# Optimization experiments

Measured on AMD Instinct MI355X. Metric: run time of the kernel, lower is better.

Reference implementation:

```python
import jax, jax.numpy as jnp
import numpy as np

Q_MAX = 127.0  # int8 symmetric quant range


def setup_inputs() -> dict:
    key = jax.random.key(0)
    kx, kw, ks = jax.random.split(key, 3)
    M, K, N = 16384, 4096, 4096
    x = jax.random.normal(kx, (M, K), dtype=jnp.float32)
    # int8 weight values in [-127, 127]
    weight = jax.random.randint(kw, (N, K), -127, 128, dtype=jnp.int32).astype(jnp.int8)
    # per-output-row dequant scale, small positive values as a real quantizer would produce
    weight_scale = jax.random.uniform(ks, (N, 1), dtype=jnp.float32, minval=1e-3, maxval=1e-2)
    return {"x": x, "weight": weight, "weight_scale": weight_scale}


def reference(x, weight, weight_scale):
    # --- per-token dynamic activation quantization (get_hip_quant(per_Token)) ---
    amax = jnp.max(jnp.abs(x), axis=-1, keepdims=True)            # [M,1]
    x_scale = amax / Q_MAX                                        # [M,1]
    x_q = jnp.clip(jnp.round(x / jnp.maximum(x_scale, 1e-8)), -Q_MAX, Q_MAX)  # int8 values, kept fp32
    # --- gemm_a8w8: int8xint8 GEMM with fused dequant (row scale_a * col scale_b) ---
    acc = jnp.einsum('mk,nk->mn', x_q, weight.astype(jnp.float32),
                     preferred_element_type=jnp.float32)          # [M,N] int accumulation in fp32
    y = acc * x_scale * weight_scale.T                            # fused dequant scales
    return y  # fp32 stand-in for otype=bf16 output
```

## Files before the change

### kernel.cpp

```cpp
#include <hip/hip_runtime.h>
#include <stdint.h>

#define M_DIM 16384
#define N_DIM 4096
#define K_DIM 4096

#define BM 256
#define BN 256
#define BK 128
#define NT (K_DIM / BK)

typedef int i32x4 __attribute__((ext_vector_type(4)));

__device__ __forceinline__ void async16(const uint8_t* g, uint8_t* l) {
    __builtin_amdgcn_global_load_lds(
        (const __attribute__((address_space(1))) void*)g,
        (__attribute__((address_space(3))) void*)l,
        16, 0, 0);
}

__global__ __launch_bounds__(256) void prep_kernel(const float* __restrict__ x,
                                                   const int* __restrict__ w32,
                                                   uint32_t* __restrict__ xq,
                                                   float* __restrict__ xscale,
                                                   uint32_t* __restrict__ w8) {
    const int b = blockIdx.x;
    const int t = threadIdx.x;
    if (b >= M_DIM) {
        const int i = (b - M_DIM) * 256 + t;
        const int4 v = reinterpret_cast<const int4*>(w32)[i];
        w8[i] = (uint32_t)(v.x & 255) | ((uint32_t)(v.y & 255) << 8) |
                ((uint32_t)(v.z & 255) << 16) | ((uint32_t)(v.w & 255) << 24);
        return;
    }
    const int m = b;
    const float4* row = reinterpret_cast<const float4*>(x + (size_t)m * K_DIM);
    float4 v[4];
    float amax = 0.0f;
#pragma unroll
    for (int i = 0; i < 4; ++i) {
        v[i] = row[t + i * 256];
        amax = fmaxf(amax, fmaxf(fmaxf(fabsf(v[i].x), fabsf(v[i].y)),
                                 fmaxf(fabsf(v[i].z), fabsf(v[i].w))));
    }
#pragma unroll
    for (int off = 32; off > 0; off >>= 1) amax = fmaxf(amax, __shfl_xor(amax, off));
    __shared__ float smax[4];
    if ((t & 63) == 0) smax[t >> 6] = amax;
    __syncthreads();
    amax = fmaxf(fmaxf(smax[0], smax[1]), fmaxf(smax[2], smax[3]));
    const float scale = amax / 127.0f;
    const float s = fmaxf(scale, 1e-8f);
    if (t == 0) xscale[m] = scale;
    uint32_t* orow = xq + (size_t)m * (K_DIM / 4);
#pragma unroll
    for (int i = 0; i < 4; ++i) {
        int q0 = __float2int_rn(v[i].x / s);
        int q1 = __float2int_rn(v[i].y / s);
        int q2 = __float2int_rn(v[i].z / s);
        int q3 = __float2int_rn(v[i].w / s);
        q0 = max(-127, min(127, q0));
        q1 = max(-127, min(127, q1));
        q2 = max(-127, min(127, q2));
        q3 = max(-127, min(127, q3));
        orow[t + i * 256] = (uint32_t)(q0 & 255) | ((uint32_t)(q1 & 255) << 8) |
                            ((uint32_t)(q2 & 255) << 16) | ((uint32_t)(q3 & 255) << 24);
    }
}

__global__ __launch_bounds__(512, 2) void gemm_kernel(
    const uint8_t* __restrict__ Aq, const float* __restrict__ ascale,
    const uint8_t* __restrict__ Bq, const float* __restrict__ wscale,
    float* __restrict__ out) {
    __shared__ uint8_t lds[4 * BM * BK];
    uint8_t* ldsA0 = lds;
    uint8_t* ldsA1 = lds + BM * BK;
    uint8_t* ldsB0 = lds + 2 * BM * BK;
    uint8_t* ldsB1 = lds + 3 * BM * BK;

    const int tid = threadIdx.x;
    const int lane = tid & 63;
    const int w = tid >> 6;
    const int wr = w >> 2;
    const int wc = w & 3;
    const int lr = lane & 15;
    const int lg = lane >> 4;

    const int bid = blockIdx.x;
    const int swz = (bid & 7) * (1024 / 8) + (bid >> 3);
    const size_t row0 = (size_t)(swz >> 4) * BM;
    const size_t col0 = (size_t)(swz & 15) * BN;
    const uint8_t* Ab = Aq + row0 * K_DIM;
    const uint8_t* Bb = Bq + col0 * K_DIM;

    i32x4 acc[8][4];
#pragma unroll
    for (int i = 0; i < 8; ++i)
#pragma unroll
        for (int j = 0; j < 4; ++j) acc[i][j] = (i32x4){0, 0, 0, 0};

#define STAGE_P(BASE, DST, KT)                                                   \
    do {                                                                         \
        _Pragma("unroll") for (int it_ = 0; it_ < 4; ++it_) {                    \
            const int idx_ = it_ * 512 + tid;                                    \
            const int m_ = idx_ >> 3, p_ = idx_ & 7;                             \
            async16((BASE) + (size_t)m_ * K_DIM + (KT) * BK +                    \
                        ((p_ ^ (m_ & 7)) << 4),                                  \
                    (DST) + (it_ * 512 + w * 64) * 16);                          \
        }                                                                        \
    } while (0)

#define READ_K(BUFA, BUFB, KK, F)                                                \
    do {                                                                         \
        _Pragma("unroll") for (int q_ = 0; q_ < 8; ++q_) {                       \
            const int r_ = wr * 128 + q_ * 16 + lr;                              \
            const int u_ = (KK) * 4 + lg;                                        \
            afk[F][q_] = *reinterpret_cast<const i32x4*>(                        \
                (BUFA) + r_ * BK + ((u_ ^ (r_ & 7)) << 4));                      \
        }                                                                        \
        _Pragma("unroll") for (int p_ = 0; p_ < 4; ++p_) {                       \
            const int r_ = wc * 64 + p_ * 16 + lr;                               \
            const int u_ = (KK) * 4 + lg;                                        \
            bfk[F][p_] = *reinterpret_cast<const i32x4*>(                        \
                (BUFB) + r_ * BK + ((u_ ^ (r_ & 7)) << 4));                      \
        }                                                                        \
    } while (0)

#define CLUSTER(F)                                                               \
    do {                                                                         \
        __builtin_amdgcn_s_setprio(1);                                           \
        _Pragma("unroll") for (int q_ = 0; q_ < 8; ++q_)                         \
        _Pragma("unroll") for (int p_ = 0; p_ < 4; ++p_)                         \
            acc[q_][p_] = __builtin_amdgcn_mfma_i32_16x16x64_i8(                 \
                afk[F][q_], bfk[F][p_], acc[q_][p_], 0, 0, 0);                   \
        __builtin_amdgcn_s_setprio(0);                                           \
    } while (0)

#define BAR __builtin_amdgcn_s_barrier()
#define VMCNT(N) asm volatile("s_waitcnt vmcnt(" #N ")" ::: "memory")
#define LGKM0                                              \
    do {                                                   \
        asm volatile("s_waitcnt lgkmcnt(0)" ::: "memory"); \
        __builtin_amdgcn_sched_barrier(0);                 \
    } while (0)

#define TILE_G0(CA, CB, NA, NB, TB, TA2)                                         \
    do {                                                                         \
        LGKM0;                                                  \
        STAGE_P(Bb, NB, TB);                                         \
        READ_K(CA, CB, 1, 1);                                            \
        CLUSTER(0);                                                              \
        LGKM0;                                                     \
        VMCNT(0);                                      \
        BAR;                                                                     \
        STAGE_P(Ab, CA, TA2);                               \
        READ_K(NA, NB, 0, 0);                                       \
        CLUSTER(1);                                                              \
    } while (0)

#define TILE_G1(CA, CB, NA, NB, TB, TA2)                                         \
    do {                                                                         \
        LGKM0;                                                                   \
        STAGE_P(Bb, NB, TB);                                                     \
        CLUSTER(0);                                                              \
        READ_K(CA, CB, 1, 1);                                                    \
        LGKM0;                                                                   \
        VMCNT(0);                                                                \
        BAR;                                                                     \
        STAGE_P(Ab, CA, TA2);                                                    \
        CLUSTER(1);                                                              \
        READ_K(NA, NB, 0, 0);                                                    \
    } while (0)

#define MAIN_LOOP(TILE_X)                                                        \
    do {                                                                         \
        READ_K(ldsA0, ldsB0, 0, 0);                                              \
        _Pragma("unroll 1") for (int it2 = 0; it2 < NT / 2; ++it2) {             \
            const int T = 2 * it2;                                               \
            const int Tp2 = (T + 2 < NT) ? T + 2 : NT - 1;                       \
            const int Tp3 = (T + 3 < NT) ? T + 3 : NT - 1;                       \
            TILE_X(ldsA0, ldsB0, ldsA1, ldsB1, T + 1, Tp2);                      \
            TILE_X(ldsA1, ldsB1, ldsA0, ldsB0, Tp2, Tp3);                        \
        }                                                                        \
    } while (0)

    i32x4 afk[2][8], bfk[2][4];

    STAGE_P(Ab, ldsA0, 0);
    STAGE_P(Bb, ldsB0, 0);
    STAGE_P(Ab, ldsA1, 1);
    VMCNT(4);
    BAR;

    if (wr == 0) {
        MAIN_LOOP(TILE_G0);
    } else {
        MAIN_LOOP(TILE_G1);
    }

    const float* asp = ascale + row0 + wr * 128;
    const float* wsp = wscale + col0 + wc * 64;
    float wsv[4];
#pragma unroll
    for (int nf = 0; nf < 4; ++nf) wsv[nf] = wsp[nf * 16 + lr];
    float* outBase = out + (row0 + wr * 128) * (size_t)N_DIM + col0 + wc * 64;
#pragma unroll
    for (int mf = 0; mf < 8; ++mf) {
#pragma unroll
        for (int j = 0; j < 4; ++j) {
            const int r = mf * 16 + lg * 4 + j;
            const float av = asp[r];
            float* orow = outBase + (size_t)r * N_DIM;
#pragma unroll
            for (int nf = 0; nf < 4; ++nf) {
                orow[nf * 16 + lr] = (float)acc[mf][nf][j] * av * wsv[nf];
            }
        }
    }
#undef STAGE_P
#undef READ_K
#undef CLUSTER
#undef TILE_G0
#undef TILE_G1
#undef MAIN_LOOP
#undef BAR
#undef VMCNT
#undef LGKM0
}

extern "C" void kernel_launch(void* const* d_in, const int* in_sizes, int n_in,
                              void* d_out, int out_size, void* d_ws, size_t ws_size,
                              hipStream_t stream) {
    const float* x = (const float*)d_in[0];
    const int* w32 = (const int*)d_in[1];
    const float* wscale = (const float*)d_in[2];
    float* out = (float*)d_out;

    uint8_t* ws = (uint8_t*)d_ws;
    uint32_t* xq = (uint32_t*)ws;
    float* xscale = (float*)(ws + (size_t)M_DIM * K_DIM);
    uint8_t* wq = ws + (size_t)M_DIM * K_DIM + (size_t)M_DIM * 4;

    prep_kernel<<<dim3(M_DIM + N_DIM * K_DIM / 4 / 256), 256, 0, stream>>>(
        x, w32, xq, xscale, (uint32_t*)wq);
    gemm_kernel<<<dim3((M_DIM / BM) * (N_DIM / BN)), 512, 0, stream>>>(
        (const uint8_t*)xq, xscale, wq, wscale, out);
}
```

Before: 341.6 us.

## Switch int8 GEMM to 32x32x32 MFMA tiles and drop redundant lgkm waits

Replaces the 16x16x64 int8 MFMA with the 32x32x32 variant, so each wave computes its 128x64 sub-tile as 4x2 32x32 blocks with 16-element accumulators. LDS fragment reads and the epilogue row/column mapping are rewritten to match the new MFMA register layout. It also removes the leading lgkmcnt(0) wait at the start of each tile stage. The larger instruction means fewer MFMA issues and fewer LDS fragment loads per K step. The cost is a changed output-store pattern, and a risk of LDS hazards from the removed wait.

```diff
diff --git a/kernel.cpp b/kernel.cpp
--- a/kernel.cpp
+++ b/kernel.cpp
@@ -11,6 +11,7 @@
 #define NT (K_DIM / BK)
 
 typedef int i32x4 __attribute__((ext_vector_type(4)));
+typedef int i32x16 __attribute__((ext_vector_type(16)));
 
 __device__ __forceinline__ void async16(const uint8_t* g, uint8_t* l) {
     __builtin_amdgcn_global_load_lds(
@@ -83,8 +84,8 @@
     const int w = tid >> 6;
     const int wr = w >> 2;
     const int wc = w & 3;
-    const int lr = lane & 15;
-    const int lg = lane >> 4;
+    const int l31 = lane & 31;
+    const int hi = lane >> 5;
 
     const int bid = blockIdx.x;
     const int swz = (bid & 7) * (1024 / 8) + (bid >> 3);
@@ -93,11 +94,11 @@
     const uint8_t* Ab = Aq + row0 * K_DIM;
     const uint8_t* Bb = Bq + col0 * K_DIM;
 
-    i32x4 acc[8][4];
-#pragma unroll
-    for (int i = 0; i < 8; ++i)
-#pragma unroll
-        for (int j = 0; j < 4; ++j) acc[i][j] = (i32x4){0, 0, 0, 0};
+    i32x16 acc[4][2];
+#pragma unroll
+    for (int i = 0; i < 4; ++i)
+#pragma unroll
+        for (int j = 0; j < 2; ++j) acc[i][j] = (i32x16)(0);
 
 #define STAGE_P(BASE, DST, KT)                                                   \
     do {                                                                         \
@@ -112,16 +113,18 @@
 
 #define READ_K(BUFA, BUFB, KK, F)                                                \
     do {                                                                         \
-        _Pragma("unroll") for (int q_ = 0; q_ < 8; ++q_) {                       \
-            const int r_ = wr * 128 + q_ * 16 + lr;                              \
-            const int u_ = (KK) * 4 + lg;                                        \
-            afk[F][q_] = *reinterpret_cast<const i32x4*>(                        \
+        _Pragma("unroll") for (int mf_ = 0; mf_ < 4; ++mf_)                      \
+        _Pragma("unroll") for (int s_ = 0; s_ < 2; ++s_) {                       \
+            const int r_ = wr * 128 + mf_ * 32 + l31;                            \
+            const int u_ = (KK) * 4 + s_ * 2 + hi;                               \
+            afk[F][mf_ * 2 + s_] = *reinterpret_cast<const i32x4*>(              \
                 (BUFA) + r_ * BK + ((u_ ^ (r_ & 7)) << 4));                      \
         }                                                                        \
-        _Pragma("unroll") for (int p_ = 0; p_ < 4; ++p_) {                       \
-            const int r_ = wc * 64 + p_ * 16 + lr;                               \
-            const int u_ = (KK) * 4 + lg;                                        \
-            bfk[F][p_] = *reinterpret_cast<const i32x4*>(                        \
+        _Pragma("unroll") for (int nh_ = 0; nh_ < 2; ++nh_)                      \
+        _Pragma("unroll") for (int s_ = 0; s_ < 2; ++s_) {                       \
+            const int r_ = wc * 64 + nh_ * 32 + l31;                             \
+            const int u_ = (KK) * 4 + s_ * 2 + hi;                               \
+            bfk[F][nh_ * 2 + s_] = *reinterpret_cast<const i32x4*>(              \
                 (BUFB) + r_ * BK + ((u_ ^ (r_ & 7)) << 4));                      \
         }                                                                        \
     } while (0)
@@ -129,10 +132,12 @@
 #define CLUSTER(F)                                                               \
     do {                                                                         \
         __builtin_amdgcn_s_setprio(1);                                           \
-        _Pragma("unroll") for (int q_ = 0; q_ < 8; ++q_)                         \
-        _Pragma("unroll") for (int p_ = 0; p_ < 4; ++p_)                         \
-            acc[q_][p_] = __builtin_amdgcn_mfma_i32_16x16x64_i8(                 \
-                afk[F][q_], bfk[F][p_], acc[q_][p_], 0, 0, 0);                   \
+        _Pragma("unroll") for (int s_ = 0; s_ < 2; ++s_)                         \
+        _Pragma("unroll") for (int mf_ = 0; mf_ < 4; ++mf_)                      \
+        _Pragma("unroll") for (int nh_ = 0; nh_ < 2; ++nh_)                      \
+            acc[mf_][nh_] = __builtin_amdgcn_mfma_i32_32x32x32_i8(               \
+                afk[F][mf_ * 2 + s_], bfk[F][nh_ * 2 + s_],                      \
+                acc[mf_][nh_], 0, 0, 0);                                         \
         __builtin_amdgcn_s_setprio(0);                                           \
     } while (0)
 
@@ -146,21 +151,19 @@
 
 #define TILE_G0(CA, CB, NA, NB, TB, TA2)                                         \
     do {                                                                         \
-        LGKM0;                                                  \
-        STAGE_P(Bb, NB, TB);                                         \
-        READ_K(CA, CB, 1, 1);                                            \
+        STAGE_P(Bb, NB, TB);                                                     \
+        READ_K(CA, CB, 1, 1);                                                    \
         CLUSTER(0);                                                              \
-        LGKM0;                                                     \
-        VMCNT(0);                                      \
+        LGKM0;                                                                   \
+        VMCNT(0);                                                                \
         BAR;                                                                     \
-        STAGE_P(Ab, CA, TA2);                               \
-        READ_K(NA, NB, 0, 0);                                       \
+        STAGE_P(Ab, CA, TA2);                                                    \
+        READ_K(NA, NB, 0, 0);                                                    \
         CLUSTER(1);                                                              \
     } while (0)
 
 #define TILE_G1(CA, CB, NA, NB, TB, TA2)                                         \
     do {                                                                         \
-        LGKM0;                                                                   \
         STAGE_P(Bb, NB, TB);                                                     \
         CLUSTER(0);                                                              \
         READ_K(CA, CB, 1, 1);                                                    \
@@ -200,20 +203,20 @@
 
     const float* asp = ascale + row0 + wr * 128;
     const float* wsp = wscale + col0 + wc * 64;
-    float wsv[4];
-#pragma unroll
-    for (int nf = 0; nf < 4; ++nf) wsv[nf] = wsp[nf * 16 + lr];
+    float wsv[2];
+#pragma unroll
+    for (int nf = 0; nf < 2; ++nf) wsv[nf] = wsp[nf * 32 + l31];
     float* outBase = out + (row0 + wr * 128) * (size_t)N_DIM + col0 + wc * 64;
 #pragma unroll
-    for (int mf = 0; mf < 8; ++mf) {
-#pragma unroll
-        for (int j = 0; j < 4; ++j) {
-            const int r = mf * 16 + lg * 4 + j;
+    for (int mf = 0; mf < 4; ++mf) {
+#pragma unroll
+        for (int j = 0; j < 16; ++j) {
+            const int r = mf * 32 + (j & 3) + 8 * (j >> 2) + 4 * hi;
             const float av = asp[r];
             float* orow = outBase + (size_t)r * N_DIM;
 #pragma unroll
-            for (int nf = 0; nf < 4; ++nf) {
-                orow[nf * 16 + lr] = (float)acc[mf][nf][j] * av * wsv[nf];
+            for (int nf = 0; nf < 2; ++nf) {
+                orow[nf * 32 + l31] = (float)acc[mf][nf][j] * av * wsv[nf];
             }
         }
     }
```

Measured after the change: 387.1 us. +13.3%, slower.
